# Optimization experiments

Measured on AMD Instinct MI355X. Metric: run time of the kernel, lower is better.

Reference implementation:

```python
import jax, jax.numpy as jnp
import numpy as np

N_CELLS = 19683   # 27**3 lattice
K = 26            # Moore-neighborhood max_neighbors
D = 128           # state_size
HG = 64           # gating hidden
CNF_STEPS = 3     # integration_steps
DT = 0.1


def setup_inputs() -> dict:
    key = jax.random.key(0)
    ks = jax.random.split(key, 12)
    s = lambda fan_in: 1.0 / np.sqrt(fan_in)
    return {
        "current_state": jax.random.normal(ks[0], (N_CELLS, D), jnp.float32),
        "neighbor_states": jax.random.normal(ks[1], (N_CELLS, K, D), jnp.float32),
        "conn_type": jax.random.randint(ks[2], (N_CELLS, K), 0, 3, jnp.int32),
        "W_local": jax.random.normal(ks[3], (2 * D, D), jnp.float32) * s(2 * D),
        "b_local": jnp.zeros((D,), jnp.float32),
        "W_msg": jax.random.normal(ks[4], (2 * D, D), jnp.float32) * s(2 * D),
        "b_msg": jnp.zeros((D,), jnp.float32),
        "W_upd": jax.random.normal(ks[5], (2 * D, D), jnp.float32) * s(2 * D),
        "b_upd": jnp.zeros((D,), jnp.float32),
        "W_cnf": jax.random.normal(ks[6], (2 * D, D), jnp.float32) * s(2 * D),
        "b_cnf": jnp.zeros((D,), jnp.float32),
        "W_g1": jax.random.normal(ks[7], (D, HG), jnp.float32) * s(D),
        "b_g1": jnp.zeros((HG,), jnp.float32),
        "W_g2": jax.random.normal(ks[8], (HG, 3), jnp.float32) * s(HG),
        "b_g2": jnp.zeros((3,), jnp.float32),
    }


def _masked_mean(nbr, mask):
    # nbr: [N,K,D], mask: [N,K] float -> [N,D]
    cnt = jnp.maximum(mask.sum(-1, keepdims=True), 1.0)
    return jnp.einsum("nkd,nk->nd", nbr, mask) / cnt


def reference(current_state, neighbor_states, conn_type,
              W_local, b_local, W_msg, b_msg, W_upd, b_upd,
              W_cnf, b_cnf, W_g1, b_g1, W_g2, b_g2):
    cur = current_state                       # [N,D]
    nbr = neighbor_states                     # [N,K,D]
    m_l = (conn_type == 0).astype(cur.dtype)  # local mask   [N,K]
    m_f = (conn_type == 1).astype(cur.dtype)  # functional
    m_d = (conn_type == 2).astype(cur.dtype)  # distant

    # --- local expert: SimpleLinear over [cell, mean(local neighbors)] ---
    agg_l = _masked_mean(nbr, m_l)
    local_out = jnp.tanh(jnp.concatenate([cur, agg_l], -1) @ W_local + b_local)

    # --- functional expert: GNN message passing ---
    cur_b = jnp.broadcast_to(cur[:, None, :], nbr.shape)          # [N,K,D]
    edge_in = jnp.concatenate([cur_b, nbr], -1)                   # [N,K,2D]
    msgs = jax.nn.relu(edge_in @ W_msg + b_msg)                   # [N,K,D]
    agg_msg = _masked_mean(msgs, m_f)                             # [N,D]
    func_out = jnp.tanh(jnp.concatenate([cur, agg_msg], -1) @ W_upd + b_upd)

    # --- distant expert: lightweight CNF (fixed-step Euler) ---
    agg_d = _masked_mean(nbr, m_d)

    def euler_step(s, _):
        ds = jnp.tanh(jnp.concatenate([s, agg_d], -1) @ W_cnf + b_cnf)
        return s + DT * ds, None

    distant_out, _ = jax.lax.scan(euler_step, cur, None, length=CNF_STEPS)

    # --- gating network: softmax over 3 experts ---
    gates = jax.nn.softmax(jax.nn.relu(cur @ W_g1 + b_g1) @ W_g2 + b_g2, -1)  # [N,3]

    out = (gates[:, 0:1] * local_out
           + gates[:, 1:2] * func_out
           + gates[:, 2:3] * distant_out)
    return out
```

## Files before the change

kernel.cpp:

```cpp
#include <hip/hip_runtime.h>
#include <hip/hip_bf16.h>
#include <math.h>

#define NC 19683
#define KN 26
#define DD 128
#define HGN 64
#define LDSB 136
#define DTC 0.1f

using bf8v = __attribute__((ext_vector_type(8))) short;
using f4v  = __attribute__((ext_vector_type(4))) float;

__device__ __forceinline__ unsigned short f2bf(float x) {
    union { float f; unsigned u; } v; v.f = x;
    unsigned r = v.u + 0x7fffu + ((v.u >> 16) & 1u);
    return (unsigned short)(r >> 16);
}
__device__ __forceinline__ unsigned pk2(float a, float b) {
    return ((unsigned)f2bf(a)) | (((unsigned)f2bf(b)) << 16);
}

__global__ __launch_bounds__(256) void k_prep(const float* __restrict__ Wl,
    const float* __restrict__ Wm, const float* __restrict__ Wu,
    const float* __restrict__ Wc, const float* __restrict__ Wg1,
    unsigned short* __restrict__ WT, unsigned short* __restrict__ WgT)
{
    int idx = blockIdx.x * 256 + threadIdx.x;
    if (idx < 131072) {
        int m = idx >> 15;
        int r = idx & 32767;
        int j = r >> 8;
        int i = r & 255;
        const float* src = (m == 0) ? Wl : (m == 1) ? Wm : (m == 2) ? Wu : Wc;
        WT[idx] = f2bf(src[i * DD + j]);
    } else {
        int idx2 = idx - 131072;
        int col = idx2 >> 7;
        int k = idx2 & 127;
        WgT[idx2] = f2bf(Wg1[k * HGN + col]);
    }
}

__global__ __launch_bounds__(256) void kB(const float* __restrict__ cur,
    const float* __restrict__ nbr, const int* __restrict__ conn,
    const unsigned short* __restrict__ WT, const float* __restrict__ b_msg,
    unsigned short* __restrict__ agg_l, unsigned short* __restrict__ agg_m,
    unsigned short* __restrict__ agg_d)
{
    __shared__ __align__(16) unsigned short Bl[128][LDSB];
    __shared__ __align__(16) unsigned short Al[4][32][LDSB];
    __shared__ float P8[4][DD];
    int t = threadIdx.x;
    int n0 = blockIdx.x * 4;
    int w = t >> 6, lane = t & 63;
    int n = n0 + w;
    bool act = n < NC;
    int lm = lane & 15, lq = lane >> 4;

    int ct = 3;
    if (act && lane < KN) ct = conn[(size_t)n * KN + lane];
    int j2 = lane * 2;
    const float* base = nbr + ((size_t)(act ? n : 0) * KN) * DD + j2;
    float2 vv[KN];
    #pragma unroll
    for (int k = 0; k < KN; ++k) {
        float2 v = {0.f, 0.f};
        if (act) v = *(const float2*)&base[(size_t)k * DD];
        vv[k] = v;
    }
    unsigned long long mlb = __ballot(ct == 0);
    unsigned long long mfb = __ballot(ct == 1);
    unsigned long long mdb = __ballot(ct == 2);
    float icl = 1.f / fmaxf((float)__builtin_popcountll(mlb), 1.f);
    float icf = 1.f / fmaxf((float)__builtin_popcountll(mfb), 1.f);
    float icd = 1.f / fmaxf((float)__builtin_popcountll(mdb), 1.f);

    const unsigned short* Wm1T = WT + 32768;
    for (int p = 0; p < 8; ++p) {
        int ch = p * 256 + t;
        int j = ch >> 4, i8 = (ch & 15) * 8;
        *(bf8v*)&Bl[j][i8] = *(const bf8v*)&Wm1T[j * 256 + i8];
    }
    {
        int r = t >> 6, c2 = (t & 63) * 2;
        float2 v = {0.f, 0.f};
        if (n0 + r < NC) v = *(const float2*)&cur[(size_t)(n0 + r) * DD + c2];
        *(unsigned*)&Al[0][r][c2] = pk2(v.x, v.y);
        unsigned* pz = (unsigned*)&Al[0][4][0];
        for (int z = t; z < 12 * LDSB / 2; z += 256) pz[z] = 0;
    }
    __syncthreads();

    for (int nt = 0; nt < 2; ++nt) {
        int col0 = w * 32 + nt * 16;
        f4v acc = {0.f, 0.f, 0.f, 0.f};
        for (int s = 0; s < 4; ++s) {
            bf8v a = *(const bf8v*)&Al[0][lm][s * 32 + lq * 8];
            bf8v b = *(const bf8v*)&Bl[col0 + lm][s * 32 + lq * 8];
            acc = __builtin_amdgcn_mfma_f32_16x16x32_bf16(a, b, acc, 0, 0, 0);
        }
        if (lq == 0) {
            int col = col0 + lm;
            float bm = b_msg[col];
            for (int r = 0; r < 4; ++r) P8[r][col] = acc[r] + bm;
        }
    }
    __syncthreads();

    const unsigned short* Wm2T = WT + 32768 + 128;
    for (int p = 0; p < 8; ++p) {
        int ch = p * 256 + t;
        int j = ch >> 4, i8 = (ch & 15) * 8;
        *(bf8v*)&Bl[j][i8] = *(const bf8v*)&Wm2T[j * 256 + i8];
    }
    float slx = 0.f, sly = 0.f, sdx = 0.f, sdy = 0.f;
    #pragma unroll
    for (int k = 0; k < KN; ++k) {
        float2 v = vv[k];
        if ((mlb >> k) & 1) { slx += v.x; sly += v.y; }
        if ((mdb >> k) & 1) { sdx += v.x; sdy += v.y; }
        *(unsigned*)&Al[w][k][j2] = pk2(v.x, v.y);
    }
    {
        unsigned* pz = (unsigned*)&Al[w][KN][0];
        for (int z = lane; z < (32 - KN) * LDSB / 2; z += 64) pz[z] = 0;
    }
    if (act) {
        *(unsigned*)&agg_l[(size_t)n * DD + j2] = pk2(slx * icl, sly * icl);
        *(unsigned*)&agg_d[(size_t)n * DD + j2] = pk2(sdx * icd, sdy * icd);
    }
    __syncthreads();

    if (act) {
        __builtin_amdgcn_s_setprio(1);
        for (int nt = 0; nt < 8; ++nt) {
            int col0 = nt * 16;
            float pv = P8[w][col0 + lm];
            float msum = 0.f;
            for (int mt2 = 0; mt2 < 2; ++mt2) {
                f4v acc = {0.f, 0.f, 0.f, 0.f};
                for (int s = 0; s < 4; ++s) {
                    bf8v a = *(const bf8v*)&Al[w][mt2 * 16 + lm][s * 32 + lq * 8];
                    bf8v b = *(const bf8v*)&Bl[col0 + lm][s * 32 + lq * 8];
                    acc = __builtin_amdgcn_mfma_f32_16x16x32_bf16(a, b, acc, 0, 0, 0);
                }
                for (int r = 0; r < 4; ++r) {
                    int row = mt2 * 16 + lq * 4 + r;
                    if ((mfb >> row) & 1) msum += fmaxf(pv + acc[r], 0.f);
                }
            }
            msum += __shfl_xor(msum, 16, 64);
            msum += __shfl_xor(msum, 32, 64);
            if (lane < 16) agg_m[(size_t)n * DD + col0 + lane] = f2bf(msum * icf);
        }
        __builtin_amdgcn_s_setprio(0);
    }
}

__global__ __launch_bounds__(256) void kC(const float* __restrict__ cur,
    const unsigned short* __restrict__ WT, const unsigned short* __restrict__ WgT,
    const unsigned short* __restrict__ agg_l, const unsigned short* __restrict__ agg_m,
    const unsigned short* __restrict__ agg_d,
    const float* __restrict__ b_local, const float* __restrict__ b_upd,
    const float* __restrict__ b_cnf, const float* __restrict__ bg1,
    const float* __restrict__ Wg2, const float* __restrict__ bg2,
    float* __restrict__ out)
{
    __shared__ __align__(16) unsigned short Wl[128][LDSB];
    __shared__ __align__(16) unsigned short Xc[32][LDSB];
    __shared__ __align__(16) unsigned short Xa[32][LDSB];
    __shared__ float hrelu[32][HGN + 4];
    __shared__ float glds[32][4];
    __shared__ float bl[DD], bu[DD], bc[DD];
    __shared__ float Wg2s[HGN * 3];
    __shared__ float bg2s[4];
    int t = threadIdx.x;
    int n0 = blockIdx.x * 32;
    int w = t >> 6, lane = t & 63;
    int mt = w & 1, colh = w >> 1;
    int lm = lane & 15, lq = lane >> 4;

    auto stageW = [&](int m, int koff) {
        const unsigned short* src = WT + m * 32768 + koff;
        for (int p = 0; p < 8; ++p) {
            int ch = p * 256 + t;
            int j = ch >> 4, i8 = (ch & 15) * 8;
            *(bf8v*)&Wl[j][i8] = *(const bf8v*)&src[j * 256 + i8];
        }
    };
    auto stageXa = [&](const unsigned short* src) {
        for (int p = 0; p < 2; ++p) {
            int idx = p * 256 + t;
            int r = idx >> 4, c8 = (idx & 15) * 8;
            bf8v v = {0, 0, 0, 0, 0, 0, 0, 0};
            if (n0 + r < NC) v = *(const bf8v*)&src[(size_t)(n0 + r) * DD + c8];
            *(bf8v*)&Xa[r][c8] = v;
        }
    };
    auto mfmaPass = [&](unsigned short (&X)[32][LDSB], f4v* acc) {
        for (int nt = 0; nt < 4; ++nt) {
            int col0 = colh * 64 + nt * 16;
            for (int s = 0; s < 4; ++s) {
                bf8v a = *(const bf8v*)&X[mt * 16 + lm][s * 32 + lq * 8];
                bf8v b = *(const bf8v*)&Wl[col0 + lm][s * 32 + lq * 8];
                acc[nt] = __builtin_amdgcn_mfma_f32_16x16x32_bf16(a, b, acc[nt], 0, 0, 0);
            }
        }
    };

    for (int p = 0; p < 8; ++p) {
        int idx = p * 256 + t;
        int r = idx >> 6, c2 = (idx & 63) * 2;
        float2 v = {0.f, 0.f};
        if (n0 + r < NC) v = *(const float2*)&cur[(size_t)(n0 + r) * DD + c2];
        *(unsigned*)&Xc[r][c2] = pk2(v.x, v.y);
    }
    for (int p = 0; p < 4; ++p) {
        int ch = p * 256 + t;
        int j = ch >> 4, i8 = (ch & 15) * 8;
        *(bf8v*)&Wl[j][i8] = *(const bf8v*)&WgT[j * 128 + i8];
    }
    if (t < 128) { bl[t] = b_local[t]; bu[t] = b_upd[t]; bc[t] = b_cnf[t]; }
    for (int i = t; i < HGN * 3; i += 256) Wg2s[i] = Wg2[i];
    if (t < 3) bg2s[t] = bg2[t];
    __syncthreads();

    {
        int col0 = w * 16;
        float bg = bg1[col0 + lm];
        for (int mt2 = 0; mt2 < 2; ++mt2) {
            f4v acc = {0.f, 0.f, 0.f, 0.f};
            for (int s = 0; s < 4; ++s) {
                bf8v a = *(const bf8v*)&Xc[mt2 * 16 + lm][s * 32 + lq * 8];
                bf8v b = *(const bf8v*)&Wl[col0 + lm][s * 32 + lq * 8];
                acc = __builtin_amdgcn_mfma_f32_16x16x32_bf16(a, b, acc, 0, 0, 0);
            }
            for (int r = 0; r < 4; ++r)
                hrelu[mt2 * 16 + lq * 4 + r][col0 + lm] = fmaxf(acc[r] + bg, 0.f);
        }
    }
    __syncthreads();

    stageW(0, 0);
    if (t < 96) {
        int r = t / 3, e = t - r * 3;
        float s = bg2s[e];
        for (int g = 0; g < HGN; ++g) s += hrelu[r][g] * Wg2s[g * 3 + e];
        glds[r][e] = s;
    }
    __syncthreads();

    if (t < 32) {
        float l0 = glds[t][0], l1 = glds[t][1], l2 = glds[t][2];
        float m = fmaxf(l0, fmaxf(l1, l2));
        float e0 = expf(l0 - m), e1 = expf(l1 - m), e2 = expf(l2 - m);
        float inv = 1.f / (e0 + e1 + e2);
        glds[t][0] = e0 * inv; glds[t][1] = e1 * inv; glds[t][2] = e2 * inv;
    }
    f4v oacc[4], acc[4];
    for (int nt = 0; nt < 4; ++nt) oacc[nt] = (f4v){0.f, 0.f, 0.f, 0.f};

    for (int nt = 0; nt < 4; ++nt) acc[nt] = (f4v){0.f, 0.f, 0.f, 0.f};
    mfmaPass(Xc, acc);
    __syncthreads();
    stageW(0, 128); stageXa(agg_l);
    __syncthreads();
    mfmaPass(Xa, acc);
    for (int nt = 0; nt < 4; ++nt) {
        int col = colh * 64 + nt * 16 + lm;
        for (int r = 0; r < 4; ++r) {
            int row = mt * 16 + lq * 4 + r;
            oacc[nt][r] += glds[row][0] * tanhf(acc[nt][r] + bl[col]);
        }
    }

    __syncthreads();
    stageW(2, 0);
    __syncthreads();
    for (int nt = 0; nt < 4; ++nt) acc[nt] = (f4v){0.f, 0.f, 0.f, 0.f};
    mfmaPass(Xc, acc);
    __syncthreads();
    stageW(2, 128); stageXa(agg_m);
    __syncthreads();
    mfmaPass(Xa, acc);
    for (int nt = 0; nt < 4; ++nt) {
        int col = colh * 64 + nt * 16 + lm;
        for (int r = 0; r < 4; ++r) {
            int row = mt * 16 + lq * 4 + r;
            oacc[nt][r] += glds[row][1] * tanhf(acc[nt][r] + bu[col]);
        }
    }

    __syncthreads();
    stageW(3, 128); stageXa(agg_d);
    __syncthreads();
    for (int nt = 0; nt < 4; ++nt) acc[nt] = (f4v){0.f, 0.f, 0.f, 0.f};
    mfmaPass(Xa, acc);
    f4v hd[4], s[4];
    for (int nt = 0; nt < 4; ++nt) {
        int col = colh * 64 + nt * 16 + lm;
        for (int r = 0; r < 4; ++r) {
            int row = mt * 16 + lq * 4 + r;
            int n = n0 + row;
            hd[nt][r] = acc[nt][r] + bc[col];
            s[nt][r] = (n < NC) ? cur[(size_t)n * DD + col] : 0.f;
        }
    }
    __syncthreads();
    stageW(3, 0);
    for (int step = 0; step < 3; ++step) {
        for (int nt = 0; nt < 4; ++nt) {
            int col = colh * 64 + nt * 16 + lm;
            for (int r = 0; r < 4; ++r) {
                int row = mt * 16 + lq * 4 + r;
                Xa[row][col] = f2bf(s[nt][r]);
            }
        }
        __syncthreads();
        for (int nt = 0; nt < 4; ++nt) acc[nt] = (f4v){0.f, 0.f, 0.f, 0.f};
        mfmaPass(Xa, acc);
        for (int nt = 0; nt < 4; ++nt)
            for (int r = 0; r < 4; ++r)
                s[nt][r] += DTC * tanhf(acc[nt][r] + hd[nt][r]);
        __syncthreads();
    }

    for (int nt = 0; nt < 4; ++nt) {
        int col = colh * 64 + nt * 16 + lm;
        for (int r = 0; r < 4; ++r) {
            int row = mt * 16 + lq * 4 + r;
            int n = n0 + row;
            if (n < NC) out[(size_t)n * DD + col] = oacc[nt][r] + glds[row][2] * s[nt][r];
        }
    }
}

extern "C" void kernel_launch(void* const* d_in, const int* in_sizes, int n_in,
                              void* d_out, int out_size, void* d_ws, size_t ws_size,
                              hipStream_t stream) {
    const float* cur     = (const float*)d_in[0];
    const float* nbr     = (const float*)d_in[1];
    const int*   conn    = (const int*)d_in[2];
    const float* W_local = (const float*)d_in[3];
    const float* b_local = (const float*)d_in[4];
    const float* W_msg   = (const float*)d_in[5];
    const float* b_msg   = (const float*)d_in[6];
    const float* W_upd   = (const float*)d_in[7];
    const float* b_upd   = (const float*)d_in[8];
    const float* W_cnf   = (const float*)d_in[9];
    const float* b_cnf   = (const float*)d_in[10];
    const float* Wg1     = (const float*)d_in[11];
    const float* bg1     = (const float*)d_in[12];
    const float* Wg2     = (const float*)d_in[13];
    const float* bg2     = (const float*)d_in[14];
    float* out = (float*)d_out;

    char* ws = (char*)d_ws;
    unsigned short* WT   = (unsigned short*)ws;
    unsigned short* WgT  = (unsigned short*)(ws + 262144);
    unsigned short* aggl = (unsigned short*)(ws + 278528);
    unsigned short* aggm = aggl + (size_t)NC * DD;
    unsigned short* aggd = aggm + (size_t)NC * DD;

    hipLaunchKernelGGL(k_prep, dim3(544), dim3(256), 0, stream, W_local, W_msg, W_upd, W_cnf, Wg1, WT, WgT);
    hipLaunchKernelGGL(kB, dim3(4921), dim3(256), 0, stream, cur, nbr, conn, WT, b_msg, aggl, aggm, aggd);
    hipLaunchKernelGGL(kC, dim3(616), dim3(256), 0, stream, cur, WT, WgT, aggl, aggm, aggd,
                       b_local, b_upd, b_cnf, bg1, Wg2, bg2, out);
}
```

Before: 473.4 us.

## Fuse neighbor aggregation and expert heads into one mega-kernel

Merges the neighbor-aggregation kernel and the expert/gating kernel into a single kernel that processes 24 cells per block. The bf16 aggregates stay in LDS instead of being written to and re-read from global memory. Weight tiles are read straight from global/L2 or held in registers (Wm2, Wcnf fragments) rather than staged through LDS with barriers, and a launch is removed. The costs are heavy register pressure from the fragment arrays, lower occupancy, and MFMA work on padded rows since 24 cells fill a 32-row tile.

```diff
diff --git a/kernel.cpp b/kernel.cpp
--- a/kernel.cpp
+++ b/kernel.cpp
@@ -1,23 +1,23 @@
 #include <hip/hip_runtime.h>
-#include <hip/hip_bf16.h>
 #include <math.h>
 
 #define NC 19683
 #define KN 26
 #define DD 128
 #define HGN 64
+#define CB 24
 #define LDSB 136
 #define DTC 0.1f
 
 using bf8v = __attribute__((ext_vector_type(8))) short;
 using f4v  = __attribute__((ext_vector_type(4))) float;
 
-__device__ __forceinline__ unsigned short f2bf(float x) {
+static __device__ __forceinline__ unsigned short f2bf(float x) {
     union { float f; unsigned u; } v; v.f = x;
     unsigned r = v.u + 0x7fffu + ((v.u >> 16) & 1u);
     return (unsigned short)(r >> 16);
 }
-__device__ __forceinline__ unsigned pk2(float a, float b) {
+static __device__ __forceinline__ unsigned pk2(float a, float b) {
     return ((unsigned)f2bf(a)) | (((unsigned)f2bf(b)) << 16);
 }
 
@@ -42,184 +42,40 @@
     }
 }
 
-__global__ __launch_bounds__(256) void kB(const float* __restrict__ cur,
-    const float* __restrict__ nbr, const int* __restrict__ conn,
-    const unsigned short* __restrict__ WT, const float* __restrict__ b_msg,
-    unsigned short* __restrict__ agg_l, unsigned short* __restrict__ agg_m,
-    unsigned short* __restrict__ agg_d)
-{
-    __shared__ __align__(16) unsigned short Bl[128][LDSB];
-    __shared__ __align__(16) unsigned short Al[4][32][LDSB];
-    __shared__ float P8[4][DD];
-    int t = threadIdx.x;
-    int n0 = blockIdx.x * 4;
-    int w = t >> 6, lane = t & 63;
-    int n = n0 + w;
-    bool act = n < NC;
-    int lm = lane & 15, lq = lane >> 4;
-
-    int ct = 3;
-    if (act && lane < KN) ct = conn[(size_t)n * KN + lane];
-    int j2 = lane * 2;
-    const float* base = nbr + ((size_t)(act ? n : 0) * KN) * DD + j2;
-    float2 vv[KN];
-    #pragma unroll
-    for (int k = 0; k < KN; ++k) {
-        float2 v = {0.f, 0.f};
-        if (act) v = *(const float2*)&base[(size_t)k * DD];
-        vv[k] = v;
-    }
-    unsigned long long mlb = __ballot(ct == 0);
-    unsigned long long mfb = __ballot(ct == 1);
-    unsigned long long mdb = __ballot(ct == 2);
-    float icl = 1.f / fmaxf((float)__builtin_popcountll(mlb), 1.f);
-    float icf = 1.f / fmaxf((float)__builtin_popcountll(mfb), 1.f);
-    float icd = 1.f / fmaxf((float)__builtin_popcountll(mdb), 1.f);
-
-    const unsigned short* Wm1T = WT + 32768;
-    for (int p = 0; p < 8; ++p) {
-        int ch = p * 256 + t;
-        int j = ch >> 4, i8 = (ch & 15) * 8;
-        *(bf8v*)&Bl[j][i8] = *(const bf8v*)&Wm1T[j * 256 + i8];
-    }
-    {
-        int r = t >> 6, c2 = (t & 63) * 2;
-        float2 v = {0.f, 0.f};
-        if (n0 + r < NC) v = *(const float2*)&cur[(size_t)(n0 + r) * DD + c2];
-        *(unsigned*)&Al[0][r][c2] = pk2(v.x, v.y);
-        unsigned* pz = (unsigned*)&Al[0][4][0];
-        for (int z = t; z < 12 * LDSB / 2; z += 256) pz[z] = 0;
-    }
-    __syncthreads();
-
-    for (int nt = 0; nt < 2; ++nt) {
-        int col0 = w * 32 + nt * 16;
-        f4v acc = {0.f, 0.f, 0.f, 0.f};
-        for (int s = 0; s < 4; ++s) {
-            bf8v a = *(const bf8v*)&Al[0][lm][s * 32 + lq * 8];
-            bf8v b = *(const bf8v*)&Bl[col0 + lm][s * 32 + lq * 8];
-            acc = __builtin_amdgcn_mfma_f32_16x16x32_bf16(a, b, acc, 0, 0, 0);
-        }
-        if (lq == 0) {
-            int col = col0 + lm;
-            float bm = b_msg[col];
-            for (int r = 0; r < 4; ++r) P8[r][col] = acc[r] + bm;
-        }
-    }
-    __syncthreads();
-
-    const unsigned short* Wm2T = WT + 32768 + 128;
-    for (int p = 0; p < 8; ++p) {
-        int ch = p * 256 + t;
-        int j = ch >> 4, i8 = (ch & 15) * 8;
-        *(bf8v*)&Bl[j][i8] = *(const bf8v*)&Wm2T[j * 256 + i8];
-    }
-    float slx = 0.f, sly = 0.f, sdx = 0.f, sdy = 0.f;
-    #pragma unroll
-    for (int k = 0; k < KN; ++k) {
-        float2 v = vv[k];
-        if ((mlb >> k) & 1) { slx += v.x; sly += v.y; }
-        if ((mdb >> k) & 1) { sdx += v.x; sdy += v.y; }
-        *(unsigned*)&Al[w][k][j2] = pk2(v.x, v.y);
-    }
-    {
-        unsigned* pz = (unsigned*)&Al[w][KN][0];
-        for (int z = lane; z < (32 - KN) * LDSB / 2; z += 64) pz[z] = 0;
-    }
-    if (act) {
-        *(unsigned*)&agg_l[(size_t)n * DD + j2] = pk2(slx * icl, sly * icl);
-        *(unsigned*)&agg_d[(size_t)n * DD + j2] = pk2(sdx * icd, sdy * icd);
-    }
-    __syncthreads();
-
-    if (act) {
-        __builtin_amdgcn_s_setprio(1);
-        for (int nt = 0; nt < 8; ++nt) {
-            int col0 = nt * 16;
-            float pv = P8[w][col0 + lm];
-            float msum = 0.f;
-            for (int mt2 = 0; mt2 < 2; ++mt2) {
-                f4v acc = {0.f, 0.f, 0.f, 0.f};
-                for (int s = 0; s < 4; ++s) {
-                    bf8v a = *(const bf8v*)&Al[w][mt2 * 16 + lm][s * 32 + lq * 8];
-                    bf8v b = *(const bf8v*)&Bl[col0 + lm][s * 32 + lq * 8];
-                    acc = __builtin_amdgcn_mfma_f32_16x16x32_bf16(a, b, acc, 0, 0, 0);
-                }
-                for (int r = 0; r < 4; ++r) {
-                    int row = mt2 * 16 + lq * 4 + r;
-                    if ((mfb >> row) & 1) msum += fmaxf(pv + acc[r], 0.f);
-                }
-            }
-            msum += __shfl_xor(msum, 16, 64);
-            msum += __shfl_xor(msum, 32, 64);
-            if (lane < 16) agg_m[(size_t)n * DD + col0 + lane] = f2bf(msum * icf);
-        }
-        __builtin_amdgcn_s_setprio(0);
-    }
-}
-
-__global__ __launch_bounds__(256) void kC(const float* __restrict__ cur,
-    const unsigned short* __restrict__ WT, const unsigned short* __restrict__ WgT,
-    const unsigned short* __restrict__ agg_l, const unsigned short* __restrict__ agg_m,
-    const unsigned short* __restrict__ agg_d,
+#define ALr(c,k) (U + ((c) * 32 + (k)) * LDSB)
+#define XCr(r)   (U + (128 + (r)) * LDSB)
+#define AGLr(r)  (U + (152 + (r)) * LDSB)
+#define AGMr(r)  (U + (176 + (r)) * LDSB)
+#define AGDr(r)  (U + (200 + (r)) * LDSB)
+
+__global__ __launch_bounds__(256, 2) void kMega(
+    const float* __restrict__ cur, const float* __restrict__ nbr,
+    const int* __restrict__ conn, const unsigned short* __restrict__ WT,
+    const unsigned short* __restrict__ WgT, const float* __restrict__ b_msg,
     const float* __restrict__ b_local, const float* __restrict__ b_upd,
     const float* __restrict__ b_cnf, const float* __restrict__ bg1,
     const float* __restrict__ Wg2, const float* __restrict__ bg2,
     float* __restrict__ out)
 {
-    __shared__ __align__(16) unsigned short Wl[128][LDSB];
-    __shared__ __align__(16) unsigned short Xc[32][LDSB];
-    __shared__ __align__(16) unsigned short Xa[32][LDSB];
-    __shared__ float hrelu[32][HGN + 4];
+    __shared__ __align__(16) unsigned short U[232 * LDSB];
+    __shared__ __align__(16) float uP[CB * DD];
     __shared__ float glds[32][4];
     __shared__ float bl[DD], bu[DD], bc[DD];
     __shared__ float Wg2s[HGN * 3];
     __shared__ float bg2s[4];
+
     int t = threadIdx.x;
-    int n0 = blockIdx.x * 32;
+    int n0 = blockIdx.x * CB;
     int w = t >> 6, lane = t & 63;
+    int lm = lane & 15, lq = lane >> 4;
     int mt = w & 1, colh = w >> 1;
-    int lm = lane & 15, lq = lane >> 4;
-
-    auto stageW = [&](int m, int koff) {
-        const unsigned short* src = WT + m * 32768 + koff;
-        for (int p = 0; p < 8; ++p) {
-            int ch = p * 256 + t;
-            int j = ch >> 4, i8 = (ch & 15) * 8;
-            *(bf8v*)&Wl[j][i8] = *(const bf8v*)&src[j * 256 + i8];
-        }
-    };
-    auto stageXa = [&](const unsigned short* src) {
-        for (int p = 0; p < 2; ++p) {
-            int idx = p * 256 + t;
-            int r = idx >> 4, c8 = (idx & 15) * 8;
-            bf8v v = {0, 0, 0, 0, 0, 0, 0, 0};
-            if (n0 + r < NC) v = *(const bf8v*)&src[(size_t)(n0 + r) * DD + c8];
-            *(bf8v*)&Xa[r][c8] = v;
-        }
-    };
-    auto mfmaPass = [&](unsigned short (&X)[32][LDSB], f4v* acc) {
-        for (int nt = 0; nt < 4; ++nt) {
-            int col0 = colh * 64 + nt * 16;
-            for (int s = 0; s < 4; ++s) {
-                bf8v a = *(const bf8v*)&X[mt * 16 + lm][s * 32 + lq * 8];
-                bf8v b = *(const bf8v*)&Wl[col0 + lm][s * 32 + lq * 8];
-                acc[nt] = __builtin_amdgcn_mfma_f32_16x16x32_bf16(a, b, acc[nt], 0, 0, 0);
-            }
-        }
-    };
-
-    for (int p = 0; p < 8; ++p) {
+
+    for (int p = 0; p < 6; ++p) {
         int idx = p * 256 + t;
         int r = idx >> 6, c2 = (idx & 63) * 2;
         float2 v = {0.f, 0.f};
         if (n0 + r < NC) v = *(const float2*)&cur[(size_t)(n0 + r) * DD + c2];
-        *(unsigned*)&Xc[r][c2] = pk2(v.x, v.y);
-    }
-    for (int p = 0; p < 4; ++p) {
-        int ch = p * 256 + t;
-        int j = ch >> 4, i8 = (ch & 15) * 8;
-        *(bf8v*)&Wl[j][i8] = *(const bf8v*)&WgT[j * 128 + i8];
+        *(unsigned*)&XCr(r)[c2] = pk2(v.x, v.y);
     }
     if (t < 128) { bl[t] = b_local[t]; bu[t] = b_upd[t]; bc[t] = b_cnf[t]; }
     for (int i = t; i < HGN * 3; i += 256) Wg2s[i] = Wg2[i];
@@ -231,42 +87,140 @@
         float bg = bg1[col0 + lm];
         for (int mt2 = 0; mt2 < 2; ++mt2) {
             f4v acc = {0.f, 0.f, 0.f, 0.f};
+            #pragma unroll
             for (int s = 0; s < 4; ++s) {
-                bf8v a = *(const bf8v*)&Xc[mt2 * 16 + lm][s * 32 + lq * 8];
-                bf8v b = *(const bf8v*)&Wl[col0 + lm][s * 32 + lq * 8];
+                bf8v a = *(const bf8v*)&XCr(mt2 * 16 + lm)[s * 32 + lq * 8];
+                bf8v b = *(const bf8v*)&WgT[(col0 + lm) * 128 + s * 32 + lq * 8];
                 acc = __builtin_amdgcn_mfma_f32_16x16x32_bf16(a, b, acc, 0, 0, 0);
             }
-            for (int r = 0; r < 4; ++r)
-                hrelu[mt2 * 16 + lq * 4 + r][col0 + lm] = fmaxf(acc[r] + bg, 0.f);
-        }
-    }
-    __syncthreads();
-
-    stageW(0, 0);
-    if (t < 96) {
+            for (int r = 0; r < 4; ++r) {
+                int row = mt2 * 16 + lq * 4 + r;
+                if (row < CB) uP[row * 68 + col0 + lm] = fmaxf(acc[r] + bg, 0.f);
+            }
+        }
+    }
+    __syncthreads();
+
+    if (t < CB * 3) {
         int r = t / 3, e = t - r * 3;
         float s = bg2s[e];
-        for (int g = 0; g < HGN; ++g) s += hrelu[r][g] * Wg2s[g * 3 + e];
+        for (int g = 0; g < HGN; ++g) s += uP[r * 68 + g] * Wg2s[g * 3 + e];
         glds[r][e] = s;
     }
     __syncthreads();
 
-    if (t < 32) {
+    {
+        const unsigned short* Wm1 = WT + 32768;
+        for (int nt = 0; nt < 2; ++nt) {
+            int col0 = w * 32 + nt * 16;
+            float bm = b_msg[col0 + lm];
+            const unsigned short* bb = &Wm1[(col0 + lm) * 256 + lq * 8];
+            for (int mt2 = 0; mt2 < 2; ++mt2) {
+                f4v acc = {0.f, 0.f, 0.f, 0.f};
+                #pragma unroll
+                for (int s = 0; s < 4; ++s) {
+                    bf8v a = *(const bf8v*)&XCr(mt2 * 16 + lm)[s * 32 + lq * 8];
+                    bf8v b = *(const bf8v*)&bb[s * 32];
+                    acc = __builtin_amdgcn_mfma_f32_16x16x32_bf16(a, b, acc, 0, 0, 0);
+                }
+                for (int r = 0; r < 4; ++r) {
+                    int row = mt2 * 16 + lq * 4 + r;
+                    if (row < CB) uP[row * DD + col0 + lm] = acc[r] + bm;
+                }
+            }
+        }
+    }
+    if (t < CB) {
         float l0 = glds[t][0], l1 = glds[t][1], l2 = glds[t][2];
         float m = fmaxf(l0, fmaxf(l1, l2));
         float e0 = expf(l0 - m), e1 = expf(l1 - m), e2 = expf(l2 - m);
         float inv = 1.f / (e0 + e1 + e2);
         glds[t][0] = e0 * inv; glds[t][1] = e1 * inv; glds[t][2] = e2 * inv;
     }
+    __syncthreads();
+
+    bf8v bfr[8][4];
+    {
+        const unsigned short* Wm2 = WT + 32768 + 128;
+        #pragma unroll
+        for (int nt = 0; nt < 8; ++nt)
+            #pragma unroll
+            for (int s = 0; s < 4; ++s)
+                bfr[nt][s] = *(const bf8v*)&Wm2[(nt * 16 + lm) * 256 + s * 32 + lq * 8];
+    }
+
+    int j2 = lane * 2;
+    for (int chv = 0; chv < 6; ++chv) {
+        int row = chv * 4 + w;
+        int n = n0 + row;
+        bool act = n < NC;
+        int ct = 3;
+        if (act && lane < KN) ct = conn[(size_t)n * KN + lane];
+        unsigned long long mlb = __ballot(ct == 0);
+        unsigned long long mfb = __ballot(ct == 1);
+        unsigned long long mdb = __ballot(ct == 2);
+        float icl = 1.f / fmaxf((float)__builtin_popcountll(mlb), 1.f);
+        float icf = 1.f / fmaxf((float)__builtin_popcountll(mfb), 1.f);
+        float icd = 1.f / fmaxf((float)__builtin_popcountll(mdb), 1.f);
+        float slx = 0.f, sly = 0.f, sdx = 0.f, sdy = 0.f;
+        const float* basep = nbr + (size_t)(act ? n : 0) * KN * DD + j2;
+        #pragma unroll
+        for (int k = 0; k < KN; ++k) {
+            float2 v = {0.f, 0.f};
+            if (act) v = *(const float2*)&basep[(size_t)k * DD];
+            if ((mlb >> k) & 1) { slx += v.x; sly += v.y; }
+            if ((mdb >> k) & 1) { sdx += v.x; sdy += v.y; }
+            *(unsigned*)&ALr(w, k)[j2] = pk2(v.x, v.y);
+        }
+        *(unsigned*)&AGLr(row)[j2] = pk2(slx * icl, sly * icl);
+        *(unsigned*)&AGDr(row)[j2] = pk2(sdx * icd, sdy * icd);
+        __builtin_amdgcn_s_setprio(1);
+        #pragma unroll
+        for (int nt = 0; nt < 8; ++nt) {
+            float pv = uP[row * DD + nt * 16 + lm];
+            float msum = 0.f;
+            #pragma unroll
+            for (int mt2 = 0; mt2 < 2; ++mt2) {
+                f4v acc = {0.f, 0.f, 0.f, 0.f};
+                #pragma unroll
+                for (int s = 0; s < 4; ++s) {
+                    bf8v a = *(const bf8v*)&ALr(w, mt2 * 16 + lm)[s * 32 + lq * 8];
+                    acc = __builtin_amdgcn_mfma_f32_16x16x32_bf16(a, bfr[nt][s], acc, 0, 0, 0);
+                }
+                #pragma unroll
+                for (int r = 0; r < 4; ++r) {
+                    int rr = mt2 * 16 + lq * 4 + r;
+                    if ((mfb >> rr) & 1) msum += fmaxf(pv + acc[r], 0.f);
+                }
+            }
+            msum += __shfl_xor(msum, 16, 64);
+            msum += __shfl_xor(msum, 32, 64);
+            if (lane < 16) AGMr(row)[nt * 16 + lane] = f2bf(msum * icf);
+        }
+        __builtin_amdgcn_s_setprio(0);
+    }
+    __syncthreads();
+
+    auto mfmaPassG = [&](const unsigned short* Xbase, int m, int koff, f4v* acc) {
+        const unsigned short* Wb = WT + m * 32768 + koff + lq * 8;
+        #pragma unroll
+        for (int nt = 0; nt < 4; ++nt) {
+            int col0 = colh * 64 + nt * 16;
+            #pragma unroll
+            for (int s = 0; s < 4; ++s) {
+                bf8v a = *(const bf8v*)&Xbase[(mt * 16 + lm) * LDSB + s * 32 + lq * 8];
+                bf8v b = *(const bf8v*)&Wb[(col0 + lm) * 256 + s * 32];
+                acc[nt] = __builtin_amdgcn_mfma_f32_16x16x32_bf16(a, b, acc[nt], 0, 0, 0);
+            }
+        }
+    };
+
     f4v oacc[4], acc[4];
     for (int nt = 0; nt < 4; ++nt) oacc[nt] = (f4v){0.f, 0.f, 0.f, 0.f};
 
     for (int nt = 0; nt < 4; ++nt) acc[nt] = (f4v){0.f, 0.f, 0.f, 0.f};
-    mfmaPass(Xc, acc);
-    __syncthreads();
-    stageW(0, 128); stageXa(agg_l);
-    __syncthreads();
-    mfmaPass(Xa, acc);
+    mfmaPassG(XCr(0), 0, 0, acc);
+    mfmaPassG(AGLr(0), 0, 128, acc);
     for (int nt = 0; nt < 4; ++nt) {
         int col = colh * 64 + nt * 16 + lm;
         for (int r = 0; r < 4; ++r) {
@@ -275,15 +229,9 @@
         }
     }
 
-    __syncthreads();
-    stageW(2, 0);
-    __syncthreads();
     for (int nt = 0; nt < 4; ++nt) acc[nt] = (f4v){0.f, 0.f, 0.f, 0.f};
-    mfmaPass(Xc, acc);
-    __syncthreads();
-    stageW(2, 128); stageXa(agg_m);
-    __syncthreads();
-    mfmaPass(Xa, acc);
+    mfmaPassG(XCr(0), 2, 0, acc);
+    mfmaPassG(AGMr(0), 2, 128, acc);
     for (int nt = 0; nt < 4; ++nt) {
         int col = colh * 64 + nt * 16 + lm;
         for (int r = 0; r < 4; ++r) {
@@ -292,37 +240,46 @@
         }
     }
 
-    __syncthreads();
-    stageW(3, 128); stageXa(agg_d);
-    __syncthreads();
     for (int nt = 0; nt < 4; ++nt) acc[nt] = (f4v){0.f, 0.f, 0.f, 0.f};
-    mfmaPass(Xa, acc);
-    f4v hd[4], s[4];
+    mfmaPassG(AGDr(0), 3, 128, acc);
+    f4v hd[4], sst[4];
     for (int nt = 0; nt < 4; ++nt) {
         int col = colh * 64 + nt * 16 + lm;
         for (int r = 0; r < 4; ++r) {
             int row = mt * 16 + lq * 4 + r;
             int n = n0 + row;
             hd[nt][r] = acc[nt][r] + bc[col];
-            s[nt][r] = (n < NC) ? cur[(size_t)n * DD + col] : 0.f;
-        }
-    }
-    __syncthreads();
-    stageW(3, 0);
+            sst[nt][r] = (row < CB && n < NC) ? cur[(size_t)n * DD + col] : 0.f;
+        }
+    }
+    bf8v cfr[4][4];
+    #pragma unroll
+    for (int nt = 0; nt < 4; ++nt)
+        #pragma unroll
+        for (int s = 0; s < 4; ++s)
+            cfr[nt][s] = *(const bf8v*)&WT[3 * 32768 + (colh * 64 + nt * 16 + lm) * 256 + s * 32 + lq * 8];
+
     for (int step = 0; step < 3; ++step) {
         for (int nt = 0; nt < 4; ++nt) {
             int col = colh * 64 + nt * 16 + lm;
             for (int r = 0; r < 4; ++r) {
                 int row = mt * 16 + lq * 4 + r;
-                Xa[row][col] = f2bf(s[nt][r]);
+                ALr(0, row)[col] = f2bf(sst[nt][r]);
             }
         }
         __syncthreads();
         for (int nt = 0; nt < 4; ++nt) acc[nt] = (f4v){0.f, 0.f, 0.f, 0.f};
-        mfmaPass(Xa, acc);
+        #pragma unroll
+        for (int nt = 0; nt < 4; ++nt) {
+            #pragma unroll
+            for (int s = 0; s < 4; ++s) {
+                bf8v a = *(const bf8v*)&ALr(0, mt * 16 + lm)[s * 32 + lq * 8];
+                acc[nt] = __builtin_amdgcn_mfma_f32_16x16x32_bf16(a, cfr[nt][s], acc[nt], 0, 0, 0);
+            }
+        }
         for (int nt = 0; nt < 4; ++nt)
             for (int r = 0; r < 4; ++r)
-                s[nt][r] += DTC * tanhf(acc[nt][r] + hd[nt][r]);
+                sst[nt][r] += DTC * tanhf(acc[nt][r] + hd[nt][r]);
         __syncthreads();
     }
 
@@ -331,7 +288,8 @@
         for (int r = 0; r < 4; ++r) {
             int row = mt * 16 + lq * 4 + r;
             int n = n0 + row;
-            if (n < NC) out[(size_t)n * DD + col] = oacc[nt][r] + glds[row][2] * s[nt][r];
+            if (row < CB && n < NC)
+                out[(size_t)n * DD + col] = oacc[nt][r] + glds[row][2] * sst[nt][r];
         }
     }
 }
@@ -357,14 +315,12 @@
     float* out = (float*)d_out;
 
     char* ws = (char*)d_ws;
-    unsigned short* WT   = (unsigned short*)ws;
-    unsigned short* WgT  = (unsigned short*)(ws + 262144);
-    unsigned short* aggl = (unsigned short*)(ws + 278528);
-    unsigned short* aggm = aggl + (size_t)NC * DD;
-    unsigned short* aggd = aggm + (size_t)NC * DD;
-
-    hipLaunchKernelGGL(k_prep, dim3(544), dim3(256), 0, stream, W_local, W_msg, W_upd, W_cnf, Wg1, WT, WgT);
-    hipLaunchKernelGGL(kB, dim3(4921), dim3(256), 0, stream, cur, nbr, conn, WT, b_msg, aggl, aggm, aggd);
-    hipLaunchKernelGGL(kC, dim3(616), dim3(256), 0, stream, cur, WT, WgT, aggl, aggm, aggd,
-                       b_local, b_upd, b_cnf, bg1, Wg2, bg2, out);
-}
+    unsigned short* WT  = (unsigned short*)ws;
+    unsigned short* WgT = (unsigned short*)(ws + 262144);
+
+    hipLaunchKernelGGL(k_prep, dim3(544), dim3(256), 0, stream,
+                       W_local, W_msg, W_upd, W_cnf, Wg1, WT, WgT);
+    hipLaunchKernelGGL(kMega, dim3((NC + CB - 1) / CB), dim3(256), 0, stream,
+                       cur, nbr, conn, WT, WgT, b_msg, b_local, b_upd, b_cnf,
+                       bg1, Wg2, bg2, out);
+}
```

Measured after the change: 598.4 us. 26.4% more time.

## Process 32 cells per block with per-wave neighbor prefetch in message kernel

Applied to the files above, without the earlier changes.

The message-passing kernel now handles 32 cells per block (8 per wave) instead of 4. The two W_msg halves are staged into LDS once per 32 cells, which cuts repeated weight traffic. The cur-side projection is done as one 32-row MFMA tile, and each wave prefetches the next cell's neighbor rows into registers while it computes the current cell. A-fragments are held in registers and reused across column tiles. The costs are higher register pressure, fewer blocks, and overlapping LDS rows between waves that hold garbage for masked rows.

```diff
diff --git a/kernel.cpp b/kernel.cpp
--- a/kernel.cpp
+++ b/kernel.cpp
@@ -1,5 +1,4 @@
 #include <hip/hip_runtime.h>
-#include <hip/hip_bf16.h>
 #include <math.h>
 
 #define NC 19683
@@ -8,16 +7,18 @@
 #define HGN 64
 #define LDSB 136
 #define DTC 0.1f
+#define CPW 8
+#define CPB 32
 
 using bf8v = __attribute__((ext_vector_type(8))) short;
 using f4v  = __attribute__((ext_vector_type(4))) float;
 
-__device__ __forceinline__ unsigned short f2bf(float x) {
+static __device__ __forceinline__ unsigned short f2bf(float x) {
     union { float f; unsigned u; } v; v.f = x;
     unsigned r = v.u + 0x7fffu + ((v.u >> 16) & 1u);
     return (unsigned short)(r >> 16);
 }
-__device__ __forceinline__ unsigned pk2(float a, float b) {
+static __device__ __forceinline__ unsigned pk2(float a, float b) {
     return ((unsigned)f2bf(a)) | (((unsigned)f2bf(b)) << 16);
 }
 
@@ -42,117 +43,148 @@
     }
 }
 
-__global__ __launch_bounds__(256) void kB(const float* __restrict__ cur,
+__global__ __launch_bounds__(256, 2) void kE(const float* __restrict__ cur,
     const float* __restrict__ nbr, const int* __restrict__ conn,
     const unsigned short* __restrict__ WT, const float* __restrict__ b_msg,
     unsigned short* __restrict__ agg_l, unsigned short* __restrict__ agg_m,
     unsigned short* __restrict__ agg_d)
 {
-    __shared__ __align__(16) unsigned short Bl[128][LDSB];
-    __shared__ __align__(16) unsigned short Al[4][32][LDSB];
-    __shared__ float P8[4][DD];
+    __shared__ __align__(16) unsigned short Wt[128 * LDSB];
+    __shared__ __align__(16) unsigned short Anb[110 * LDSB];
+    __shared__ float Pbuf[CPB * DD];
     int t = threadIdx.x;
-    int n0 = blockIdx.x * 4;
+    int n0 = blockIdx.x * CPB;
     int w = t >> 6, lane = t & 63;
-    int n = n0 + w;
-    bool act = n < NC;
     int lm = lane & 15, lq = lane >> 4;
-
-    int ct = 3;
-    if (act && lane < KN) ct = conn[(size_t)n * KN + lane];
     int j2 = lane * 2;
-    const float* base = nbr + ((size_t)(act ? n : 0) * KN) * DD + j2;
-    float2 vv[KN];
-    #pragma unroll
-    for (int k = 0; k < KN; ++k) {
-        float2 v = {0.f, 0.f};
-        if (act) v = *(const float2*)&base[(size_t)k * DD];
-        vv[k] = v;
-    }
-    unsigned long long mlb = __ballot(ct == 0);
-    unsigned long long mfb = __ballot(ct == 1);
-    unsigned long long mdb = __ballot(ct == 2);
-    float icl = 1.f / fmaxf((float)__builtin_popcountll(mlb), 1.f);
-    float icf = 1.f / fmaxf((float)__builtin_popcountll(mfb), 1.f);
-    float icd = 1.f / fmaxf((float)__builtin_popcountll(mdb), 1.f);
-
-    const unsigned short* Wm1T = WT + 32768;
+
     for (int p = 0; p < 8; ++p) {
-        int ch = p * 256 + t;
-        int j = ch >> 4, i8 = (ch & 15) * 8;
-        *(bf8v*)&Bl[j][i8] = *(const bf8v*)&Wm1T[j * 256 + i8];
-    }
-    {
-        int r = t >> 6, c2 = (t & 63) * 2;
+        int idx = p * 256 + t;
+        int r = idx >> 6, c2 = (idx & 63) * 2;
         float2 v = {0.f, 0.f};
         if (n0 + r < NC) v = *(const float2*)&cur[(size_t)(n0 + r) * DD + c2];
-        *(unsigned*)&Al[0][r][c2] = pk2(v.x, v.y);
-        unsigned* pz = (unsigned*)&Al[0][4][0];
-        for (int z = t; z < 12 * LDSB / 2; z += 256) pz[z] = 0;
-    }
-    __syncthreads();
+        *(unsigned*)&Anb[r * LDSB + c2] = pk2(v.x, v.y);
+    }
+    {
+        const unsigned short* Wm1 = WT + 32768;
+        for (int p = 0; p < 8; ++p) {
+            int ch = p * 256 + t;
+            int j = ch >> 4, i8 = (ch & 15) * 8;
+            *(bf8v*)&Wt[j * LDSB + i8] = *(const bf8v*)&Wm1[j * 256 + i8];
+        }
+    }
+    __syncthreads();
+
+    int cw0 = n0 + w * CPW;
+    float2 vv[KN];
+    int ct = 3;
+    {
+        bool a = cw0 < NC;
+        if (a && lane < KN) ct = conn[(size_t)cw0 * KN + lane];
+        const float* bp = nbr + (size_t)(a ? cw0 : 0) * KN * DD + j2;
+        #pragma unroll
+        for (int k = 0; k < KN; ++k) {
+            float2 v = {0.f, 0.f};
+            if (a) v = *(const float2*)&bp[(size_t)k * DD];
+            vv[k] = v;
+        }
+    }
 
     for (int nt = 0; nt < 2; ++nt) {
         int col0 = w * 32 + nt * 16;
-        f4v acc = {0.f, 0.f, 0.f, 0.f};
-        for (int s = 0; s < 4; ++s) {
-            bf8v a = *(const bf8v*)&Al[0][lm][s * 32 + lq * 8];
-            bf8v b = *(const bf8v*)&Bl[col0 + lm][s * 32 + lq * 8];
-            acc = __builtin_amdgcn_mfma_f32_16x16x32_bf16(a, b, acc, 0, 0, 0);
-        }
-        if (lq == 0) {
-            int col = col0 + lm;
-            float bm = b_msg[col];
-            for (int r = 0; r < 4; ++r) P8[r][col] = acc[r] + bm;
-        }
-    }
-    __syncthreads();
-
-    const unsigned short* Wm2T = WT + 32768 + 128;
-    for (int p = 0; p < 8; ++p) {
-        int ch = p * 256 + t;
-        int j = ch >> 4, i8 = (ch & 15) * 8;
-        *(bf8v*)&Bl[j][i8] = *(const bf8v*)&Wm2T[j * 256 + i8];
-    }
-    float slx = 0.f, sly = 0.f, sdx = 0.f, sdy = 0.f;
-    #pragma unroll
-    for (int k = 0; k < KN; ++k) {
-        float2 v = vv[k];
-        if ((mlb >> k) & 1) { slx += v.x; sly += v.y; }
-        if ((mdb >> k) & 1) { sdx += v.x; sdy += v.y; }
-        *(unsigned*)&Al[w][k][j2] = pk2(v.x, v.y);
-    }
+        float bm = b_msg[col0 + lm];
+        for (int mt2 = 0; mt2 < 2; ++mt2) {
+            f4v acc = {0.f, 0.f, 0.f, 0.f};
+            #pragma unroll
+            for (int s = 0; s < 4; ++s) {
+                bf8v a = *(const bf8v*)&Anb[(mt2 * 16 + lm) * LDSB + s * 32 + lq * 8];
+                bf8v b = *(const bf8v*)&Wt[(col0 + lm) * LDSB + s * 32 + lq * 8];
+                acc = __builtin_amdgcn_mfma_f32_16x16x32_bf16(a, b, acc, 0, 0, 0);
+            }
+            for (int r = 0; r < 4; ++r) {
+                int row = mt2 * 16 + lq * 4 + r;
+                Pbuf[row * DD + col0 + lm] = acc[r] + bm;
+            }
+        }
+    }
+    __syncthreads();
+
     {
-        unsigned* pz = (unsigned*)&Al[w][KN][0];
-        for (int z = lane; z < (32 - KN) * LDSB / 2; z += 64) pz[z] = 0;
-    }
-    if (act) {
+        const unsigned short* Wm2 = WT + 32768 + 128;
+        for (int p = 0; p < 8; ++p) {
+            int ch = p * 256 + t;
+            int j = ch >> 4, i8 = (ch & 15) * 8;
+            *(bf8v*)&Wt[j * LDSB + i8] = *(const bf8v*)&Wm2[j * 256 + i8];
+        }
+    }
+    __syncthreads();
+
+    int abase = w * KN;
+    for (int i = 0; i < CPW; ++i) {
+        int n = cw0 + i;
+        if (n >= NC) break;
+        unsigned long long mlb = __ballot(ct == 0);
+        unsigned long long mfb = __ballot(ct == 1);
+        unsigned long long mdb = __ballot(ct == 2);
+        float icl = 1.f / fmaxf((float)__builtin_popcountll(mlb), 1.f);
+        float icf = 1.f / fmaxf((float)__builtin_popcountll(mfb), 1.f);
+        float icd = 1.f / fmaxf((float)__builtin_popcountll(mdb), 1.f);
+        float slx = 0.f, sly = 0.f, sdx = 0.f, sdy = 0.f;
+        #pragma unroll
+        for (int k = 0; k < KN; ++k) {
+            float2 v = vv[k];
+            if ((mlb >> k) & 1) { slx += v.x; sly += v.y; }
+            if ((mdb >> k) & 1) { sdx += v.x; sdy += v.y; }
+            *(unsigned*)&Anb[(abase + k) * LDSB + j2] = pk2(v.x, v.y);
+        }
         *(unsigned*)&agg_l[(size_t)n * DD + j2] = pk2(slx * icl, sly * icl);
         *(unsigned*)&agg_d[(size_t)n * DD + j2] = pk2(sdx * icd, sdy * icd);
-    }
-    __syncthreads();
-
-    if (act) {
+
+        if (i + 1 < CPW) {
+            int n2 = cw0 + i + 1;
+            bool a2 = n2 < NC;
+            int ct2 = 3;
+            if (a2 && lane < KN) ct2 = conn[(size_t)n2 * KN + lane];
+            const float* bp2 = nbr + (size_t)(a2 ? n2 : 0) * KN * DD + j2;
+            #pragma unroll
+            for (int k = 0; k < KN; ++k) {
+                float2 v = {0.f, 0.f};
+                if (a2) v = *(const float2*)&bp2[(size_t)k * DD];
+                vv[k] = v;
+            }
+            ct = ct2;
+        }
+
+        bf8v afr[2][4];
+        #pragma unroll
+        for (int mt2 = 0; mt2 < 2; ++mt2)
+            #pragma unroll
+            for (int s = 0; s < 4; ++s)
+                afr[mt2][s] = *(const bf8v*)&Anb[(abase + mt2 * 16 + lm) * LDSB + s * 32 + lq * 8];
+
+        int prow = (w * CPW + i) * DD;
         __builtin_amdgcn_s_setprio(1);
+        #pragma unroll
         for (int nt = 0; nt < 8; ++nt) {
-            int col0 = nt * 16;
-            float pv = P8[w][col0 + lm];
+            float pv = Pbuf[prow + nt * 16 + lm];
+            f4v a0 = {0.f, 0.f, 0.f, 0.f}, a1 = {0.f, 0.f, 0.f, 0.f};
+            #pragma unroll
+            for (int s = 0; s < 4; ++s) {
+                bf8v b = *(const bf8v*)&Wt[(nt * 16 + lm) * LDSB + s * 32 + lq * 8];
+                a0 = __builtin_amdgcn_mfma_f32_16x16x32_bf16(afr[0][s], b, a0, 0, 0, 0);
+                a1 = __builtin_amdgcn_mfma_f32_16x16x32_bf16(afr[1][s], b, a1, 0, 0, 0);
+            }
             float msum = 0.f;
-            for (int mt2 = 0; mt2 < 2; ++mt2) {
-                f4v acc = {0.f, 0.f, 0.f, 0.f};
-                for (int s = 0; s < 4; ++s) {
-                    bf8v a = *(const bf8v*)&Al[w][mt2 * 16 + lm][s * 32 + lq * 8];
-                    bf8v b = *(const bf8v*)&Bl[col0 + lm][s * 32 + lq * 8];
-                    acc = __builtin_amdgcn_mfma_f32_16x16x32_bf16(a, b, acc, 0, 0, 0);
-                }
-                for (int r = 0; r < 4; ++r) {
-                    int row = mt2 * 16 + lq * 4 + r;
-                    if ((mfb >> row) & 1) msum += fmaxf(pv + acc[r], 0.f);
-                }
+            #pragma unroll
+            for (int r = 0; r < 4; ++r) {
+                int rr = lq * 4 + r;
+                if ((mfb >> rr) & 1) msum += fmaxf(pv + a0[r], 0.f);
+                int rr2 = 16 + lq * 4 + r;
+                if ((mfb >> rr2) & 1) msum += fmaxf(pv + a1[r], 0.f);
             }
             msum += __shfl_xor(msum, 16, 64);
             msum += __shfl_xor(msum, 32, 64);
-            if (lane < 16) agg_m[(size_t)n * DD + col0 + lane] = f2bf(msum * icf);
+            if (lane < 16) agg_m[(size_t)n * DD + nt * 16 + lane] = f2bf(msum * icf);
         }
         __builtin_amdgcn_s_setprio(0);
     }
@@ -363,8 +395,10 @@
     unsigned short* aggm = aggl + (size_t)NC * DD;
     unsigned short* aggd = aggm + (size_t)NC * DD;
 
-    hipLaunchKernelGGL(k_prep, dim3(544), dim3(256), 0, stream, W_local, W_msg, W_upd, W_cnf, Wg1, WT, WgT);
-    hipLaunchKernelGGL(kB, dim3(4921), dim3(256), 0, stream, cur, nbr, conn, WT, b_msg, aggl, aggm, aggd);
+    hipLaunchKernelGGL(k_prep, dim3(544), dim3(256), 0, stream,
+                       W_local, W_msg, W_upd, W_cnf, Wg1, WT, WgT);
+    hipLaunchKernelGGL(kE, dim3((NC + CPB - 1) / CPB), dim3(256), 0, stream,
+                       cur, nbr, conn, WT, b_msg, aggl, aggm, aggd);
     hipLaunchKernelGGL(kC, dim3(616), dim3(256), 0, stream, cur, WT, WgT, aggl, aggm, aggd,
                        b_local, b_upd, b_cnf, bg1, Wg2, bg2, out);
 }
```

Result: no change. 472.2 us (-0.2%).
